# Kernel tuning notes

Hardware: AMD Instinct MI355X
Metric: run time of the kernel (lower is better)

The kernel has to match this reference:

```python
import jax, jax.numpy as jnp
import numpy as np

B = 16          # patients
V = 30          # max_visit
NV = 1501       # num_nodes + 1 (node vocab incl. padding)
NE = 2001       # num_edges + 1 (relation vocab incl. padding)
H = 128         # hidden_dim
D = 128         # start_embed_dim
L = 2           # gnn layers
OUT = 25        # out_dim
N_TOTAL = 100000  # concatenated graph nodes
E = 800000        # concatenated graph edges
DECAY = 0.01
EPS = 0.0       # self_attn


def setup_inputs() -> dict:
    key = jax.random.key(0)
    ks = jax.random.split(key, 16)
    s = 0.02
    return dict(
        node_emb_w=jax.random.normal(ks[0], (NV, D), jnp.float32) * s,
        edge_emb_w=jax.random.normal(ks[1], (NE, D), jnp.float32) * s,
        lin_w=jax.random.normal(ks[2], (H, D), jnp.float32) * s,
        lin_b=jnp.zeros((H,), jnp.float32),
        alpha_w=jax.random.normal(ks[3], (L, NV, NV), jnp.float32) * 0.01,
        alpha_b=jnp.zeros((L, NV), jnp.float32),
        beta_w=jax.random.normal(ks[4], (L, 1, NV), jnp.float32) * 0.01,
        beta_b=jnp.zeros((L, 1), jnp.float32),
        wr_w=jax.random.normal(ks[5], (L, 1, H), jnp.float32) * s,
        wr_b=jnp.zeros((L, 1), jnp.float32),
        conv_w=jax.random.normal(ks[6], (L, H, H), jnp.float32) * s,
        conv_b=jnp.zeros((L, H), jnp.float32),
        mlp_w=jax.random.normal(ks[7], (OUT, 2 * H), jnp.float32) * s,
        mlp_b=jnp.zeros((OUT,), jnp.float32),
        visit_node=jax.random.randint(ks[8], (B, V, NV), 0, 2).astype(jnp.int32),
        ehr_nodes=jax.random.randint(ks[9], (B, NV), 0, 2).astype(jnp.int32),
        cat_node_ids=jax.random.randint(ks[10], (N_TOTAL,), 1, NV).astype(jnp.int32),
        cat_edge_ids=jax.random.randint(ks[11], (E,), 1, NE).astype(jnp.int32),
        edge_index=jax.random.randint(ks[12], (2, E), 0, N_TOTAL).astype(jnp.int32),
        batch=jnp.repeat(jnp.arange(B, dtype=jnp.int32), N_TOTAL // B),
    )


def reference(node_emb_w, edge_emb_w, lin_w, lin_b, alpha_w, alpha_b,
              beta_w, beta_b, wr_w, wr_b, conv_w, conv_b, mlp_w, mlp_b,
              visit_node, ehr_nodes, cat_node_ids, cat_edge_ids, edge_index, batch):
    # lambda_j = exp(decay * (max_visit - j)), shape [1, V, 1]
    lam = jnp.exp(DECAY * (V - jnp.arange(V, dtype=jnp.float32)))[None, :, None]
    # embedding lookup + shared linear projection
    x = node_emb_w[cat_node_ids] @ lin_w.T + lin_b          # [N_total, H]
    eattr = edge_emb_w[cat_edge_ids] @ lin_w.T + lin_b      # [E, H]
    vn = visit_node.astype(jnp.float32)                     # [B, V, NV]
    src, dst = edge_index[0], edge_index[1]
    xj_nid = cat_node_ids[src]                               # [E]
    xj_b = batch[src]                                        # [E]
    for l in range(L):
        # visit-level attention: softmax over visits (dim=1)
        alpha = jax.nn.softmax(vn @ alpha_w[l].T + alpha_b[l], axis=1)   # [B,V,NV]
        beta = jnp.tanh(vn @ beta_w[l].T + beta_b[l]) * lam              # [B,V,1]
        attn = jnp.sum(alpha * beta, axis=1)                              # [B,NV]
        e_attn = attn[xj_b, xj_nid][:, None]                              # [E,1] per-edge gather
        # BiAttentionGNNConv: message = relu(x_j * attn * sigmoid(W_R e)), aggr=add
        w_rel = jax.nn.sigmoid(eattr @ wr_w[l].T + wr_b[l])               # [E,1]
        msg = jax.nn.relu(x[src] * e_attn * w_rel)                        # [E,H]
        agg = jax.ops.segment_sum(msg, dst, num_segments=N_TOTAL)        # scatter-add
        x = jax.nn.relu((agg + (1.0 + EPS) * x) @ conv_w[l].T + conv_b[l])
    # global mean pool over batch segments
    counts = jax.ops.segment_sum(jnp.ones((N_TOTAL,), jnp.float32), batch, num_segments=B)
    x_graph = jax.ops.segment_sum(x, batch, num_segments=B) / counts[:, None]
    # node branch: multi-hot average of node embeddings, then shared lin
    ehr = ehr_nodes.astype(jnp.float32)
    x_node = (ehr @ node_emb_w) / jnp.sum(ehr, axis=1, keepdims=True)
    x_node = x_node @ lin_w.T + lin_b
    return jnp.concatenate([x_graph, x_node], axis=1) @ mlp_w.T + mlp_b  # [B, OUT]
```

## Files before the change

### kernel.cpp

```cpp
#include <hip/hip_runtime.h>
#include <math.h>

namespace {
constexpr int kB = 16, kV = 30, kNV = 1501, kNE = 2001, kH = 128, kD = 128,
              kL = 2, kOut = 25, kNT = 100000, kE = 800000, kM = kB * kV;
constexpr int kKP = 1504;
constexpr int kKSZ = 4;
constexpr int kNVZ = 1536;
constexpr int kMZ = 512;
constexpr int kCAP = 32;
constexpr int kWrelBlocks = (kL * kNE + 255) / 256;
constexpr int kFuseB = kWrelBlocks + kMZ;
constexpr int kFuseTotal = kFuseB + kKP * kL;
}

typedef __attribute__((ext_vector_type(8))) short bfrag;
typedef __attribute__((ext_vector_type(4))) float ffrag;

__device__ inline unsigned short f2bf(float x) {
  unsigned u = __float_as_uint(x);
  unsigned r = u + 0x7FFFu + ((u >> 16) & 1u);
  return (unsigned short)(r >> 16);
}
__device__ inline float bf2f(unsigned short h) {
  return __uint_as_float(((unsigned)h) << 16);
}

__global__ void pn_kernel(const float* __restrict__ emb, const float* __restrict__ lw,
                          const float* __restrict__ lb, const float* __restrict__ cw,
                          const float* __restrict__ cb, float* __restrict__ pn,
                          float* __restrict__ pq2, float* __restrict__ ps,
                          float* __restrict__ accz) {
  int n = blockIdx.x, h = threadIdx.x;
  if (n == 0) {
    for (int i = h; i < 4128; i += kH) accz[i] = 0.f;
  }
  __shared__ float erow[kD];
  __shared__ float row[kD];
  erow[h] = emb[(size_t)n * kD + h];
  __syncthreads();
  float acc = lb[h];
#pragma unroll 8
  for (int d = 0; d < kD; d++) acc += erow[d] * lw[h * kD + d];
  pn[(size_t)n * kH + h] = acc;
  row[h] = acc;
  __syncthreads();
  float ap = 0.f, am = 0.f, aps = cb[h];
  const float* wr = cw + h * kD;
#pragma unroll 8
  for (int d = 0; d < kD; d++) {
    float r = row[d];
    float w = wr[d];
    ap = fmaf(fmaxf(r, 0.f), w, ap);
    am = fmaf(fmaxf(-r, 0.f), w, am);
    aps = fmaf(r, w, aps);
  }
  pq2[(size_t)n * kH + h] = ap;
  pq2[(size_t)(kNV + n) * kH + h] = am;
  ps[(size_t)n * kH + h] = aps;
}

__global__ void xnode_kernel(const int* __restrict__ ehr, const float* __restrict__ pn,
                             float* __restrict__ xacc, int* __restrict__ cnte) {
  int b = blockIdx.x;
  int c = blockIdx.y;
  int h = threadIdx.x;
  int n0 = c * 128;
  __shared__ int flags[128];
  int gn = n0 + h;
  flags[h] = (gn < kNV) ? ehr[(size_t)b * kNV + gn] : 0;
  __syncthreads();
  float acc = 0.f;
  int cnt = 0;
  int n1 = min(n0 + 128, kNV);
  for (int n = n0; n < n1; ++n) {
    if (flags[n - n0]) {
      acc += pn[(size_t)n * kH + h];
      cnt++;
    }
  }
  atomicAdd(&xacc[b * kH + h], acc);
  if (h == 0) atomicAdd(&cnte[b], cnt);
}

__global__ void front_kernel(const float* __restrict__ eemb, const float* __restrict__ wrw,
                             const float* __restrict__ wrb, const float* __restrict__ lw,
                             const float* __restrict__ lb, float* __restrict__ wrel,
                             const int* __restrict__ vn, short* __restrict__ out,
                             int* __restrict__ curz, const int* __restrict__ batch,
                             int* __restrict__ cnt, const float* __restrict__ bw,
                             const float* __restrict__ bb, float* __restrict__ beta,
                             const float* __restrict__ aw, short* __restrict__ awh) {
  const int blk = blockIdx.x;
  const int tid = threadIdx.x;
  if (blk < kWrelBlocks) {
    __shared__ float uc[258];
    {
      int l = tid >> 7, d = tid & 127;
      float s = 0.f;
      for (int h = 0; h < kH; h++) s += wrw[l * kH + h] * lw[h * kD + d];
      uc[tid] = s;
      if (tid < kL) {
        float c = wrb[tid];
        for (int h = 0; h < kH; h++) c += wrw[tid * kH + h] * lb[h];
        uc[256 + tid] = c;
      }
    }
    __syncthreads();
    int idx = blk * 256 + tid;
    if (idx >= kL * kNE) return;
    int l = idx / kNE, r = idx % kNE;
    float z = uc[256 + l];
    const float* u = uc + l * 128;
    const float* er = eemb + (size_t)r * kD;
    for (int d = 0; d < kD; d++) z += er[d] * u[d];
    wrel[idx] = 1.f / (1.f + expf(-z));
  } else if (blk < kFuseB) {
    int m = blk - kWrelBlocks;
    int b = m >> 5, v = m & 31;
    int gidx = m * 256 + tid;
    for (int i = gidx; i < 200000; i += 512 * 256) curz[i] = 0;
    __shared__ int bh[kB];
    __shared__ float rs[2][256];
    if (tid < kB) bh[tid] = 0;
    __syncthreads();
    if (gidx < kNT) atomicAdd(&bh[batch[gidx]], 1);
    __syncthreads();
    if (tid < kB && bh[tid]) atomicAdd(&cnt[tid], bh[tid]);
    float s0 = 0.f, s1 = 0.f;
    for (int k = tid; k < kKP; k += 256) {
      int val = (v < kV && k < kNV) ? vn[((size_t)(b * kV + v)) * kNV + k] : 0;
      out[(size_t)m * kKP + k] = val ? (short)0x3F80 : (short)0;
      if (val) {
        s0 += bw[k];
        s1 += bw[kNV + k];
      }
    }
    rs[0][tid] = s0;
    rs[1][tid] = s1;
    __syncthreads();
    for (int o = 128; o > 0; o >>= 1) {
      if (tid < o) {
        rs[0][tid] += rs[0][tid + o];
        rs[1][tid] += rs[1][tid + o];
      }
      __syncthreads();
    }
    if (tid == 0 && v < kV) {
      float lam = expf(0.01f * (float)(kV - v));
      beta[b * kV + v] = tanhf(rs[0][0] + bb[0]) * lam;
      beta[kM + b * kV + v] = tanhf(rs[1][0] + bb[1]) * lam;
    }
  } else {
    int id = blk - kFuseB;
    int n = id % kKP;
    int l = id / kKP;
    const size_t pl = (size_t)kKP * kKP;
    size_t rowo = ((size_t)l * kKP + n) * kKP;
    for (int k = tid; k < kKP; k += 256) {
      float x = (n < kNV && k < kNV) ? aw[((size_t)l * kNV + n) * kNV + k] : 0.f;
      unsigned short h1 = f2bf(x);
      float r1 = x - bf2f(h1);
      unsigned short h2 = f2bf(r1);
      float r2 = r1 - bf2f(h2);
      unsigned short h3 = f2bf(r2);
      awh[rowo + k] = (short)h1;
      awh[2 * pl + rowo + k] = (short)h2;
      awh[4 * pl + rowo + k] = (short)h3;
    }
  }
}

__global__ void zmfma_kernel(const short* __restrict__ vnbf, const short* __restrict__ awh,
                             float* __restrict__ zp) {
  const int l = blockIdx.z >> 2, ks = blockIdx.z & 3;
  const int wv = threadIdx.x >> 6, lane = threadIdx.x & 63;
  const int m0 = (blockIdx.y * 4 + wv) * 64;
  const int n0 = blockIdx.x * 32;
  const int lrow = lane & 15;
  const int koff = (lane >> 4) * 8;
  const size_t pl = (size_t)kKP * kKP;
  const short* p0 = awh + ((size_t)0 * 2 + l) * pl;
  const short* p1 = awh + ((size_t)1 * 2 + l) * pl;
  const short* p2 = awh + ((size_t)2 * 2 + l) * pl;
  ffrag acc[4][2];
#pragma unroll
  for (int i = 0; i < 4; ++i)
#pragma unroll
    for (int j = 0; j < 2; ++j) acc[i][j] = ffrag{0.f, 0.f, 0.f, 0.f};
  const int ct0 = ks * 12;
  const int ct1 = min(ct0 + 12, 47);
  for (int kt = ct0; kt < ct1; ++kt) {
    const int k = kt * 32 + koff;
    bfrag a0 = *(const bfrag*)(vnbf + (size_t)(m0 + 0 * 16 + lrow) * kKP + k);
    bfrag a1 = *(const bfrag*)(vnbf + (size_t)(m0 + 1 * 16 + lrow) * kKP + k);
    bfrag a2 = *(const bfrag*)(vnbf + (size_t)(m0 + 2 * 16 + lrow) * kKP + k);
    bfrag a3 = *(const bfrag*)(vnbf + (size_t)(m0 + 3 * 16 + lrow) * kKP + k);
    {
      bfrag b0 = *(const bfrag*)(p0 + (size_t)(n0 + lrow) * kKP + k);
      bfrag b1 = *(const bfrag*)(p0 + (size_t)(n0 + 16 + lrow) * kKP + k);
      acc[0][0] = __builtin_amdgcn_mfma_f32_16x16x32_bf16(a0, b0, acc[0][0], 0, 0, 0);
      acc[1][0] = __builtin_amdgcn_mfma_f32_16x16x32_bf16(a1, b0, acc[1][0], 0, 0, 0);
      acc[2][0] = __builtin_amdgcn_mfma_f32_16x16x32_bf16(a2, b0, acc[2][0], 0, 0, 0);
      acc[3][0] = __builtin_amdgcn_mfma_f32_16x16x32_bf16(a3, b0, acc[3][0], 0, 0, 0);
      acc[0][1] = __builtin_amdgcn_mfma_f32_16x16x32_bf16(a0, b1, acc[0][1], 0, 0, 0);
      acc[1][1] = __builtin_amdgcn_mfma_f32_16x16x32_bf16(a1, b1, acc[1][1], 0, 0, 0);
      acc[2][1] = __builtin_amdgcn_mfma_f32_16x16x32_bf16(a2, b1, acc[2][1], 0, 0, 0);
      acc[3][1] = __builtin_amdgcn_mfma_f32_16x16x32_bf16(a3, b1, acc[3][1], 0, 0, 0);
    }
    {
      bfrag b0 = *(const bfrag*)(p1 + (size_t)(n0 + lrow) * kKP + k);
      bfrag b1 = *(const bfrag*)(p1 + (size_t)(n0 + 16 + lrow) * kKP + k);
      acc[0][0] = __builtin_amdgcn_mfma_f32_16x16x32_bf16(a0, b0, acc[0][0], 0, 0, 0);
      acc[1][0] = __builtin_amdgcn_mfma_f32_16x16x32_bf16(a1, b0, acc[1][0], 0, 0, 0);
      acc[2][0] = __builtin_amdgcn_mfma_f32_16x16x32_bf16(a2, b0, acc[2][0], 0, 0, 0);
      acc[3][0] = __builtin_amdgcn_mfma_f32_16x16x32_bf16(a3, b0, acc[3][0], 0, 0, 0);
      acc[0][1] = __builtin_amdgcn_mfma_f32_16x16x32_bf16(a0, b1, acc[0][1], 0, 0, 0);
      acc[1][1] = __builtin_amdgcn_mfma_f32_16x16x32_bf16(a1, b1, acc[1][1], 0, 0, 0);
      acc[2][1] = __builtin_amdgcn_mfma_f32_16x16x32_bf16(a2, b1, acc[2][1], 0, 0, 0);
      acc[3][1] = __builtin_amdgcn_mfma_f32_16x16x32_bf16(a3, b1, acc[3][1], 0, 0, 0);
    }
    {
      bfrag b0 = *(const bfrag*)(p2 + (size_t)(n0 + lrow) * kKP + k);
      bfrag b1 = *(const bfrag*)(p2 + (size_t)(n0 + 16 + lrow) * kKP + k);
      acc[0][0] = __builtin_amdgcn_mfma_f32_16x16x32_bf16(a0, b0, acc[0][0], 0, 0, 0);
      acc[1][0] = __builtin_amdgcn_mfma_f32_16x16x32_bf16(a1, b0, acc[1][0], 0, 0, 0);
      acc[2][0] = __builtin_amdgcn_mfma_f32_16x16x32_bf16(a2, b0, acc[2][0], 0, 0, 0);
      acc[3][0] = __builtin_amdgcn_mfma_f32_16x16x32_bf16(a3, b0, acc[3][0], 0, 0, 0);
      acc[0][1] = __builtin_amdgcn_mfma_f32_16x16x32_bf16(a0, b1, acc[0][1], 0, 0, 0);
      acc[1][1] = __builtin_amdgcn_mfma_f32_16x16x32_bf16(a1, b1, acc[1][1], 0, 0, 0);
      acc[2][1] = __builtin_amdgcn_mfma_f32_16x16x32_bf16(a2, b1, acc[2][1], 0, 0, 0);
      acc[3][1] = __builtin_amdgcn_mfma_f32_16x16x32_bf16(a3, b1, acc[3][1], 0, 0, 0);
    }
  }
  const int drow0 = (lane >> 4) * 4;
  float* zb = zp + (size_t)(ks * kL + l) * kMZ * kNVZ;
#pragma unroll
  for (int i = 0; i < 4; ++i) {
    int mrow = m0 + i * 16 + drow0;
#pragma unroll
    for (int j = 0; j < 2; ++j) {
      int ncol = n0 + j * 16 + lrow;
#pragma unroll
      for (int r = 0; r < 4; ++r) zb[(size_t)(mrow + r) * kNVZ + ncol] = acc[i][j][r];
    }
  }
}

__global__ void zsm_kernel(const float* __restrict__ zp, const float* __restrict__ beta,
                           float* __restrict__ attn) {
  int idx = blockIdx.x * blockDim.x + threadIdx.x;
  if (idx >= kL * kB * kNV) return;
  int n = idx % kNV;
  int lb_ = idx / kNV;
  int l = lb_ / kB, b = lb_ % kB;
  const size_t PSTR = (size_t)kL * kMZ * kNVZ;
  const float* p = zp + ((size_t)l * kMZ + b * 32) * kNVZ + n;
  float zz[kV];
  float m = -1e30f;
#pragma unroll
  for (int v = 0; v < kV; ++v) {
    size_t o = (size_t)v * kNVZ;
    float s = p[o] + p[o + PSTR] + p[o + 2 * PSTR] + p[o + 3 * PSTR];
    zz[v] = s;
    m = fmaxf(m, s);
  }
  float s = 0.f, num = 0.f;
  const float* bet = beta + lb_ * kV;
#pragma unroll
  for (int v = 0; v < kV; ++v) {
    float e = expf(zz[v] - m);
    s += e;
    num += e * bet[v];
  }
  attn[idx] = num / s;
}

__global__ void scatter_kernel(const int* __restrict__ ei, const int* __restrict__ nid,
                               const int* __restrict__ eid, const int* __restrict__ batch,
                               const float* __restrict__ attn, const float* __restrict__ wrel,
                               int* __restrict__ cnt1, unsigned short* __restrict__ csnb,
                               float* __restrict__ cs0b, int* __restrict__ cnt2,
                               int* __restrict__ csrs2b, float* __restrict__ cs1cb) {
  int e = blockIdx.x * blockDim.x + threadIdx.x;
  if (e >= kE) return;
  int s = ei[e], d = ei[kE + e];
  int b = batch[s], n = nid[s], r = eid[e];
  float a0 = attn[(size_t)b * kNV + n];
  float a1 = attn[(size_t)kB * kNV + b * kNV + n];
  float w0 = wrel[r], w1 = wrel[kNE + r];
  int pos = atomicAdd(&cnt1[d], 1);
  if (pos < kCAP) {
    csnb[(size_t)d * kCAP + pos] = (unsigned short)(n + ((a0 > 0.f) ? 0 : kNV));
    cs0b[(size_t)d * kCAP + pos] = fabsf(a0) * w0;
  }
  if (a1 > 0.f) {
    int p2 = atomicAdd(&cnt2[d], 1);
    if (p2 < kCAP) {
      csrs2b[(size_t)d * kCAP + p2] = s;
      cs1cb[(size_t)d * kCAP + p2] = a1 * w1;
    }
  }
}

#define GACC(A, V, C)                                  \
  A.x = fmaf(V.x, C, A.x); A.y = fmaf(V.y, C, A.y);    \
  A.z = fmaf(V.z, C, A.z); A.w = fmaf(V.w, C, A.w);

__global__ void l1_kernel(const float* __restrict__ pq2, const float* __restrict__ psTab,
                          const int* __restrict__ nid, const unsigned short* __restrict__ csn,
                          const float* __restrict__ cs0, const int* __restrict__ cnt1,
                          float* __restrict__ xa) {
  const int tid = threadIdx.x;
  const int lane = tid & 63;
  const int sub = lane >> 5, sl = lane & 31;
  const int hw = (tid >> 6) * 2 + sub;
  int node = blockIdx.x * 16 + hw;
  if (node >= kNT) return;
  const float4* x4 = (const float4*)pq2;
  float4 a0 = ((const float4*)psTab)[(size_t)nid[node] * 32 + sl];
  float4 a1 = {0.f, 0.f, 0.f, 0.f};
  float4 a2 = {0.f, 0.f, 0.f, 0.f};
  float4 a3 = {0.f, 0.f, 0.f, 0.f};
  int j0 = node * kCAP;
  int j1 = j0 + min(cnt1[node], kCAP);
  for (int base = j0; base < j1; base += 32) {
    int n = j1 - base;
    if (n > 32) n = 32;
    int sidx = 0;
    float ssc = 0.f;
    if (sl < n) {
      sidx = (int)csn[base + sl];
      ssc = cs0[base + sl];
    }
    int t = 0;
    for (; t + 8 <= n; t += 8) {
      int s0 = __shfl(sidx, sub * 32 + t + 0, 64);
      int s1 = __shfl(sidx, sub * 32 + t + 1, 64);
      int s2 = __shfl(sidx, sub * 32 + t + 2, 64);
      int s3 = __shfl(sidx, sub * 32 + t + 3, 64);
      int s4i = __shfl(sidx, sub * 32 + t + 4, 64);
      int s5 = __shfl(sidx, sub * 32 + t + 5, 64);
      int s6 = __shfl(sidx, sub * 32 + t + 6, 64);
      int s7 = __shfl(sidx, sub * 32 + t + 7, 64);
      float c0 = __shfl(ssc, sub * 32 + t + 0, 64);
      float c1 = __shfl(ssc, sub * 32 + t + 1, 64);
      float c2 = __shfl(ssc, sub * 32 + t + 2, 64);
      float c3 = __shfl(ssc, sub * 32 + t + 3, 64);
      float c4 = __shfl(ssc, sub * 32 + t + 4, 64);
      float c5 = __shfl(ssc, sub * 32 + t + 5, 64);
      float c6 = __shfl(ssc, sub * 32 + t + 6, 64);
      float c7 = __shfl(ssc, sub * 32 + t + 7, 64);
      float4 v0 = x4[(size_t)s0 * 32 + sl];
      float4 v1 = x4[(size_t)s1 * 32 + sl];
      float4 v2 = x4[(size_t)s2 * 32 + sl];
      float4 v3 = x4[(size_t)s3 * 32 + sl];
      float4 v4 = x4[(size_t)s4i * 32 + sl];
      float4 v5 = x4[(size_t)s5 * 32 + sl];
      float4 v6 = x4[(size_t)s6 * 32 + sl];
      float4 v7 = x4[(size_t)s7 * 32 + sl];
      GACC(a0, v0, c0);
      GACC(a1, v1, c1);
      GACC(a2, v2, c2);
      GACC(a3, v3, c3);
      GACC(a0, v4, c4);
      GACC(a1, v5, c5);
      GACC(a2, v6, c6);
      GACC(a3, v7, c7);
    }
    for (; t + 4 <= n; t += 4) {
      int s0 = __shfl(sidx, sub * 32 + t + 0, 64);
      int s1 = __shfl(sidx, sub * 32 + t + 1, 64);
      int s2 = __shfl(sidx, sub * 32 + t + 2, 64);
      int s3 = __shfl(sidx, sub * 32 + t + 3, 64);
      float c0 = __shfl(ssc, sub * 32 + t + 0, 64);
      float c1 = __shfl(ssc, sub * 32 + t + 1, 64);
      float c2 = __shfl(ssc, sub * 32 + t + 2, 64);
      float c3 = __shfl(ssc, sub * 32 + t + 3, 64);
      float4 v0 = x4[(size_t)s0 * 32 + sl];
      float4 v1 = x4[(size_t)s1 * 32 + sl];
      float4 v2 = x4[(size_t)s2 * 32 + sl];
      float4 v3 = x4[(size_t)s3 * 32 + sl];
      GACC(a0, v0, c0);
      GACC(a1, v1, c1);
      GACC(a2, v2, c2);
      GACC(a3, v3, c3);
    }
    for (; t < n; ++t) {
      int s = __shfl(sidx, sub * 32 + t, 64);
      float sc = __shfl(ssc, sub * 32 + t, 64);
      float4 xv = x4[(size_t)s * 32 + sl];
      GACC(a0, xv, sc);
    }
  }
  float4 o;
  o.x = fmaxf(a0.x + a1.x + a2.x + a3.x, 0.f);
  o.y = fmaxf(a0.y + a1.y + a2.y + a3.y, 0.f);
  o.z = fmaxf(a0.z + a1.z + a2.z + a3.z, 0.f);
  o.w = fmaxf(a0.w + a1.w + a2.w + a3.w, 0.f);
  ((float4*)xa)[(size_t)node * 32 + sl] = o;
}

template <int POOL>
__global__ void gconv_kernel(const float* __restrict__ srcTab,
                             const float* __restrict__ selfTab,
                             const int* __restrict__ cidx, const float* __restrict__ cscal,
                             const int* __restrict__ cnt, const int* __restrict__ selfIdx,
                             const float* __restrict__ w, const float* __restrict__ bias,
                             float* __restrict__ xout, float* __restrict__ xg,
                             const int* __restrict__ batch) {
  const int nb = blockIdx.x * 64;
  const int tid = threadIdx.x;
  __shared__ float As[128 * 64];
  __shared__ float Ws[32 * 132];
  const int wv = tid >> 6;
  const int lane = tid & 63;
  const int sub = lane >> 5, sl = lane & 31;
  const int hw = wv * 2 + sub;
  const float4* x4 = (const float4*)srcTab;
  const float4* s4 = (const float4*)selfTab;
  int nct[4];
  float4 selfa[4];
#pragma unroll
  for (int p = 0; p < 4; ++p) {
    int node = nb + p * 16 + hw;
    if (node < kNT) {
      nct[p] = min(cnt[node], kCAP);
      int selfRow = selfIdx ? selfIdx[node] : node;
      selfa[p] = s4[(size_t)selfRow * 32 + sl];
    } else {
      nct[p] = 0;
      selfa[p] = float4{0.f, 0.f, 0.f, 0.f};
    }
  }
  int sidxr[4];
  float sscr[4];
#pragma unroll
  for (int p = 0; p < 4; ++p) {
    int node = nb + p * 16 + hw;
    sidxr[p] = 0;
    sscr[p] = 0.f;
    if (node < kNT && sl < nct[p]) {
      size_t jb = (size_t)node * kCAP;
      sidxr[p] = cidx[jb + sl];
      sscr[p] = cscal[jb + sl];
    }
  }
#pragma unroll
  for (int p = 0; p < 4; ++p) {
    int nl = p * 16 + hw;
    int node = nb + nl;
    if (node < kNT) {
      float4 a0 = selfa[p];
      float4 a1 = {0.f, 0.f, 0.f, 0.f};
      float4 a2 = {0.f, 0.f, 0.f, 0.f};
      float4 a3 = {0.f, 0.f, 0.f, 0.f};
      int n = nct[p];
      int sidx = sidxr[p];
      float ssc = sscr[p];
      int t = 0;
      for (; t + 8 <= n; t += 8) {
        int s0 = __shfl(sidx, sub * 32 + t + 0, 64);
        int s1 = __shfl(sidx, sub * 32 + t + 1, 64);
        int s2 = __shfl(sidx, sub * 32 + t + 2, 64);
        int s3 = __shfl(sidx, sub * 32 + t + 3, 64);
        int s4i = __shfl(sidx, sub * 32 + t + 4, 64);
        int s5 = __shfl(sidx, sub * 32 + t + 5, 64);
        int s6 = __shfl(sidx, sub * 32 + t + 6, 64);
        int s7 = __shfl(sidx, sub * 32 + t + 7, 64);
        float c0 = __shfl(ssc, sub * 32 + t + 0, 64);
        float c1 = __shfl(ssc, sub * 32 + t + 1, 64);
        float c2 = __shfl(ssc, sub * 32 + t + 2, 64);
        float c3 = __shfl(ssc, sub * 32 + t + 3, 64);
        float c4 = __shfl(ssc, sub * 32 + t + 4, 64);
        float c5 = __shfl(ssc, sub * 32 + t + 5, 64);
        float c6 = __shfl(ssc, sub * 32 + t + 6, 64);
        float c7 = __shfl(ssc, sub * 32 + t + 7, 64);
        float4 v0 = x4[(size_t)s0 * 32 + sl];
        float4 v1 = x4[(size_t)s1 * 32 + sl];
        float4 v2 = x4[(size_t)s2 * 32 + sl];
        float4 v3 = x4[(size_t)s3 * 32 + sl];
        float4 v4 = x4[(size_t)s4i * 32 + sl];
        float4 v5 = x4[(size_t)s5 * 32 + sl];
        float4 v6 = x4[(size_t)s6 * 32 + sl];
        float4 v7 = x4[(size_t)s7 * 32 + sl];
        GACC(a0, v0, c0);
        GACC(a1, v1, c1);
        GACC(a2, v2, c2);
        GACC(a3, v3, c3);
        GACC(a0, v4, c4);
        GACC(a1, v5, c5);
        GACC(a2, v6, c6);
        GACC(a3, v7, c7);
      }
      for (; t + 4 <= n; t += 4) {
        int s0 = __shfl(sidx, sub * 32 + t + 0, 64);
        int s1 = __shfl(sidx, sub * 32 + t + 1, 64);
        int s2 = __shfl(sidx, sub * 32 + t + 2, 64);
        int s3 = __shfl(sidx, sub * 32 + t + 3, 64);
        float c0 = __shfl(ssc, sub * 32 + t + 0, 64);
        float c1 = __shfl(ssc, sub * 32 + t + 1, 64);
        float c2 = __shfl(ssc, sub * 32 + t + 2, 64);
        float c3 = __shfl(ssc, sub * 32 + t + 3, 64);
        float4 v0 = x4[(size_t)s0 * 32 + sl];
        float4 v1 = x4[(size_t)s1 * 32 + sl];
        float4 v2 = x4[(size_t)s2 * 32 + sl];
        float4 v3 = x4[(size_t)s3 * 32 + sl];
        GACC(a0, v0, c0);
        GACC(a1, v1, c1);
        GACC(a2, v2, c2);
        GACC(a3, v3, c3);
      }
      for (; t < n; ++t) {
        int s = __shfl(sidx, sub * 32 + t, 64);
        float sc = __shfl(ssc, sub * 32 + t, 64);
        float4 xv = x4[(size_t)s * 32 + sl];
        GACC(a0, xv, sc);
      }
      float av[4] = {a0.x + a1.x + a2.x + a3.x, a0.y + a1.y + a2.y + a3.y,
                     a0.z + a1.z + a2.z + a3.z, a0.w + a1.w + a2.w + a3.w};
#pragma unroll
      for (int j = 0; j < 4; ++j) {
        int d = sl * 4 + j;
        int g = (nl >> 2) ^ (sl & 15);
        As[d * 64 + (g << 2) + (nl & 3)] = av[j];
      }
    }
  }
  __syncthreads();
  const int tx = tid & 31, ty = tid >> 5;
  const int n0 = tx * 4;
  float acc[4][4] = {};
  for (int kc = 0; kc < 4; ++kc) {
    if (kc) __syncthreads();
#pragma unroll
    for (int i = 0; i < 2; ++i) {
      int fi = tid + i * 512;
      int hh = fi >> 3, c4 = (fi & 7) * 4;
      float4 v = *(const float4*)(w + (size_t)hh * kD + kc * 32 + c4);
      Ws[(c4 + 0) * 132 + hh] = v.x;
      Ws[(c4 + 1) * 132 + hh] = v.y;
      Ws[(c4 + 2) * 132 + hh] = v.z;
      Ws[(c4 + 3) * 132 + hh] = v.w;
    }
    __syncthreads();
#pragma unroll
    for (int dd = 0; dd < 32; ++dd) {
      int d = kc * 32 + dd;
      float4 a = *(const float4*)&As[d * 64 + ((ty ^ ((d >> 2) & 15)) << 2)];
      float4 b0 = *(const float4*)&Ws[dd * 132 + n0];
      float am[4] = {a.x, a.y, a.z, a.w};
      float bn[4] = {b0.x, b0.y, b0.z, b0.w};
#pragma unroll
      for (int i2 = 0; i2 < 4; ++i2)
#pragma unroll
        for (int j2 = 0; j2 < 4; ++j2) acc[i2][j2] += am[i2] * bn[j2];
    }
  }
  float4 bv0 = *(const float4*)(bias + n0);
  float bb[4] = {bv0.x, bv0.y, bv0.z, bv0.w};
  if (POOL == 0) {
#pragma unroll
    for (int i2 = 0; i2 < 4; ++i2) {
      int r = nb + ty * 4 + i2;
      if (r < kNT) {
        float4 o0;
        o0.x = fmaxf(acc[i2][0] + bb[0], 0.f);
        o0.y = fmaxf(acc[i2][1] + bb[1], 0.f);
        o0.z = fmaxf(acc[i2][2] + bb[2], 0.f);
        o0.w = fmaxf(acc[i2][3] + bb[3], 0.f);
        *(float4*)(xout + (size_t)r * kH + n0) = o0;
      }
    }
  } else {
    int rlast = min(nb + 63, kNT - 1);
    int b0 = batch[nb], b1v = batch[rlast];
    if (b0 == b1v) {
      float p[4] = {};
#pragma unroll
      for (int i2 = 0; i2 < 4; ++i2) {
        int r = nb + ty * 4 + i2;
        if (r < kNT) {
#pragma unroll
          for (int j2 = 0; j2 < 4; ++j2) p[j2] += fmaxf(acc[i2][j2] + bb[j2], 0.f);
        }
      }
      __syncthreads();
      float* Ls = Ws;
#pragma unroll
      for (int j2 = 0; j2 < 4; ++j2) Ls[ty * 132 + n0 + j2] = p[j2];
      __syncthreads();
      if (tid < 128) {
        float s = 0.f;
#pragma unroll
        for (int r2 = 0; r2 < 16; ++r2) s += Ls[r2 * 132 + tid];
        atomicAdd(&xg[b0 * kH + tid], s);
      }
    } else {
#pragma unroll
      for (int i2 = 0; i2 < 4; ++i2) {
        int r = nb + ty * 4 + i2;
        if (r < kNT) {
          int br = batch[r];
#pragma unroll
          for (int j2 = 0; j2 < 4; ++j2)
            atomicAdd(&xg[br * kH + n0 + j2], fmaxf(acc[i2][j2] + bb[j2], 0.f));
        }
      }
    }
  }
}

__global__ void final_kernel(const float* __restrict__ xg, const int* __restrict__ cnt,
                             const float* __restrict__ xacc, const int* __restrict__ cnte,
                             const float* __restrict__ mw, const float* __restrict__ mb,
                             float* __restrict__ out) {
  int idx = blockIdx.x * blockDim.x + threadIdx.x;
  if (idx >= kB * kOut) return;
  int b = idx / kOut, o = idx % kOut;
  float invg = 1.f / (float)cnt[b];
  float invn = 1.f / (float)cnte[b];
  float acc = mb[o];
  const float* w = mw + (size_t)o * (2 * kH);
  for (int h = 0; h < kH; h++) acc += xg[b * kH + h] * invg * w[h];
  for (int h = 0; h < kH; h++) acc += xacc[b * kH + h] * invn * w[kH + h];
  out[idx] = acc;
}

extern "C" void kernel_launch(void* const* d_in, const int* in_sizes, int n_in,
                              void* d_out, int out_size, void* d_ws, size_t ws_size,
                              hipStream_t stream) {
  const float* node_emb = (const float*)d_in[0];
  const float* edge_emb = (const float*)d_in[1];
  const float* lin_w = (const float*)d_in[2];
  const float* lin_b = (const float*)d_in[3];
  const float* alpha_w = (const float*)d_in[4];
  const float* alpha_b = (const float*)d_in[5];
  const float* beta_w = (const float*)d_in[6];
  const float* beta_b = (const float*)d_in[7];
  const float* wr_w = (const float*)d_in[8];
  const float* wr_b = (const float*)d_in[9];
  const float* conv_w = (const float*)d_in[10];
  const float* conv_b = (const float*)d_in[11];
  const float* mlp_w = (const float*)d_in[12];
  const float* mlp_b = (const float*)d_in[13];
  const int* visit_node = (const int*)d_in[14];
  const int* ehr_nodes = (const int*)d_in[15];
  const int* cat_node_ids = (const int*)d_in[16];
  const int* cat_edge_ids = (const int*)d_in[17];
  const int* edge_index = (const int*)d_in[18];
  const int* batch = (const int*)d_in[19];

  char* ws = (char*)d_ws;
  float* ZP = (float*)(ws);
  float* XA = (float*)(ws);
  float* PN = (float*)(ws + 51200000);
  short* VNBF = (short*)(ws + 52000000);
  float* PQ2 = (float*)(ws + 53600000);
  float* PS = (float*)(ws + 55200000);
  short* AWH = (short*)(ws + 56000000);
  unsigned short* CSNB = (unsigned short*)(ws + 56000000);
  float* CS0B = (float*)(ws + 62400000);
  float* ATTN = (float*)(ws + 83200000);
  float* BETA = (float*)(ws + 83400000);
  float* WREL = (float*)(ws + 83410000);
  int* CNT1 = (int*)(ws + 83500000);
  int* CNT2 = (int*)(ws + 83900000);
  int* CSRS2B = (int*)(ws + 84300000);
  float* CS1CB = (float*)(ws + 97100000);
  float* XG = (float*)(ws + 109900000);
  int* CNT = (int*)(ws + 109908192);
  float* XNACC = (float*)(ws + 109908256);
  int* CNTE = (int*)(ws + 109916448);

  pn_kernel<<<kNV, kH, 0, stream>>>(node_emb, lin_w, lin_b, conv_w, conv_b, PN, PQ2, PS, XG);
  xnode_kernel<<<dim3(kB, 12), kH, 0, stream>>>(ehr_nodes, PN, XNACC, CNTE);
  front_kernel<<<kFuseTotal, 256, 0, stream>>>(edge_emb, wr_w, wr_b, lin_w, lin_b, WREL,
                                               visit_node, VNBF, CNT1, batch, CNT, beta_w,
                                               beta_b, BETA, alpha_w, AWH);
  zmfma_kernel<<<dim3(47, 2, kL * kKSZ), 256, 0, stream>>>(VNBF, AWH, ZP);
  zsm_kernel<<<(kL * kB * kNV + 255) / 256, 256, 0, stream>>>(ZP, BETA, ATTN);

  scatter_kernel<<<(kE + 255) / 256, 256, 0, stream>>>(edge_index, cat_node_ids, cat_edge_ids,
                                                       batch, ATTN, WREL, CNT1, CSNB, CS0B,
                                                       CNT2, CSRS2B, CS1CB);

  l1_kernel<<<(kNT + 15) / 16, 512, 0, stream>>>(PQ2, PS, cat_node_ids, CSNB, CS0B, CNT1, XA);
  gconv_kernel<1><<<(kNT + 63) / 64, 512, 0, stream>>>(XA, XA, CSRS2B, CS1CB, CNT2, nullptr,
                                                       conv_w + (size_t)kH * kD, conv_b + kH,
                                                       nullptr, XG, batch);

  final_kernel<<<2, 256, 0, stream>>>(XG, CNT, XNACC, CNTE, mlp_w, mlp_b, (float*)d_out);
}
```

Before: 293.0 us.

## Fold pn and xnode kernels into front kernel and reassociate node branch

Moves the per-node projection (pq2/ps) and the node-branch multi-hot sum into extra block ranges of the front kernel, removing two launches and the PN buffer. The node branch now sums raw embeddings and applies lin_w through a precomputed mlp_w·lin_w product in the final kernel. Partial sums are stored per block instead of accumulated atomically. The batch histogram moves into extra blocks of the zsm kernel. This removes launch overhead and serialization but changes the floating-point summation order.

```diff
diff --git a/kernel.cpp b/kernel.cpp
--- a/kernel.cpp
+++ b/kernel.cpp
@@ -10,8 +10,17 @@
 constexpr int kMZ = 512;
 constexpr int kCAP = 32;
 constexpr int kWrelBlocks = (kL * kNE + 255) / 256;
-constexpr int kFuseB = kWrelBlocks + kMZ;
-constexpr int kFuseTotal = kFuseB + kKP * kL;
+constexpr int kVnBase = kWrelBlocks;
+constexpr int kAwBase = kVnBase + kMZ;
+constexpr int kPnBase = kAwBase + kKP * kL;
+constexpr int kPnBlocks = (kNV + 1) / 2;
+constexpr int kXnBase = kPnBase + kPnBlocks;
+constexpr int kXnBlocks = kB * 12;
+constexpr int kMwBase = kXnBase + kXnBlocks;
+constexpr int kMwBlocks = (kOut * kD + 255) / 256;
+constexpr int kFrontTotal = kMwBase + kMwBlocks;
+constexpr int kZsmBlocks = (kL * kB * kNV + 255) / 256;
+constexpr int kCntBlocks = (kNT + 255) / 256;
 }
 
 typedef __attribute__((ext_vector_type(8))) short bfrag;
@@ -26,71 +35,20 @@
   return __uint_as_float(((unsigned)h) << 16);
 }
 
-__global__ void pn_kernel(const float* __restrict__ emb, const float* __restrict__ lw,
-                          const float* __restrict__ lb, const float* __restrict__ cw,
-                          const float* __restrict__ cb, float* __restrict__ pn,
-                          float* __restrict__ pq2, float* __restrict__ ps,
-                          float* __restrict__ accz) {
-  int n = blockIdx.x, h = threadIdx.x;
-  if (n == 0) {
-    for (int i = h; i < 4128; i += kH) accz[i] = 0.f;
-  }
-  __shared__ float erow[kD];
-  __shared__ float row[kD];
-  erow[h] = emb[(size_t)n * kD + h];
-  __syncthreads();
-  float acc = lb[h];
-#pragma unroll 8
-  for (int d = 0; d < kD; d++) acc += erow[d] * lw[h * kD + d];
-  pn[(size_t)n * kH + h] = acc;
-  row[h] = acc;
-  __syncthreads();
-  float ap = 0.f, am = 0.f, aps = cb[h];
-  const float* wr = cw + h * kD;
-#pragma unroll 8
-  for (int d = 0; d < kD; d++) {
-    float r = row[d];
-    float w = wr[d];
-    ap = fmaf(fmaxf(r, 0.f), w, ap);
-    am = fmaf(fmaxf(-r, 0.f), w, am);
-    aps = fmaf(r, w, aps);
-  }
-  pq2[(size_t)n * kH + h] = ap;
-  pq2[(size_t)(kNV + n) * kH + h] = am;
-  ps[(size_t)n * kH + h] = aps;
-}
-
-__global__ void xnode_kernel(const int* __restrict__ ehr, const float* __restrict__ pn,
-                             float* __restrict__ xacc, int* __restrict__ cnte) {
-  int b = blockIdx.x;
-  int c = blockIdx.y;
-  int h = threadIdx.x;
-  int n0 = c * 128;
-  __shared__ int flags[128];
-  int gn = n0 + h;
-  flags[h] = (gn < kNV) ? ehr[(size_t)b * kNV + gn] : 0;
-  __syncthreads();
-  float acc = 0.f;
-  int cnt = 0;
-  int n1 = min(n0 + 128, kNV);
-  for (int n = n0; n < n1; ++n) {
-    if (flags[n - n0]) {
-      acc += pn[(size_t)n * kH + h];
-      cnt++;
-    }
-  }
-  atomicAdd(&xacc[b * kH + h], acc);
-  if (h == 0) atomicAdd(&cnte[b], cnt);
-}
-
 __global__ void front_kernel(const float* __restrict__ eemb, const float* __restrict__ wrw,
                              const float* __restrict__ wrb, const float* __restrict__ lw,
                              const float* __restrict__ lb, float* __restrict__ wrel,
                              const int* __restrict__ vn, short* __restrict__ out,
-                             int* __restrict__ curz, const int* __restrict__ batch,
-                             int* __restrict__ cnt, const float* __restrict__ bw,
+                             int* __restrict__ curz, const float* __restrict__ bw,
                              const float* __restrict__ bb, float* __restrict__ beta,
-                             const float* __restrict__ aw, short* __restrict__ awh) {
+                             const float* __restrict__ aw, short* __restrict__ awh,
+                             const float* __restrict__ emb, const float* __restrict__ cw,
+                             const float* __restrict__ cb, float* __restrict__ pq2,
+                             float* __restrict__ ps, const int* __restrict__ ehr,
+                             float* __restrict__ xnpart, int* __restrict__ cntep,
+                             const float* __restrict__ mw, float* __restrict__ mlpw2,
+                             float* __restrict__ lbdot, float* __restrict__ xg,
+                             int* __restrict__ cntg) {
   const int blk = blockIdx.x;
   const int tid = threadIdx.x;
   if (blk < kWrelBlocks) {
@@ -115,18 +73,16 @@
     const float* er = eemb + (size_t)r * kD;
     for (int d = 0; d < kD; d++) z += er[d] * u[d];
     wrel[idx] = 1.f / (1.f + expf(-z));
-  } else if (blk < kFuseB) {
-    int m = blk - kWrelBlocks;
+  } else if (blk < kAwBase) {
+    int m = blk - kVnBase;
     int b = m >> 5, v = m & 31;
     int gidx = m * 256 + tid;
     for (int i = gidx; i < 200000; i += 512 * 256) curz[i] = 0;
-    __shared__ int bh[kB];
+    if (m == 0) {
+      for (int i = tid; i < kB * kH; i += 256) xg[i] = 0.f;
+      if (tid < kB) cntg[tid] = 0;
+    }
     __shared__ float rs[2][256];
-    if (tid < kB) bh[tid] = 0;
-    __syncthreads();
-    if (gidx < kNT) atomicAdd(&bh[batch[gidx]], 1);
-    __syncthreads();
-    if (tid < kB && bh[tid]) atomicAdd(&cnt[tid], bh[tid]);
     float s0 = 0.f, s1 = 0.f;
     for (int k = tid; k < kKP; k += 256) {
       int val = (v < kV && k < kNV) ? vn[((size_t)(b * kV + v)) * kNV + k] : 0;
@@ -151,8 +107,8 @@
       beta[b * kV + v] = tanhf(rs[0][0] + bb[0]) * lam;
       beta[kM + b * kV + v] = tanhf(rs[1][0] + bb[1]) * lam;
     }
-  } else {
-    int id = blk - kFuseB;
+  } else if (blk < kPnBase) {
+    int id = blk - kAwBase;
     int n = id % kKP;
     int l = id / kKP;
     const size_t pl = (size_t)kKP * kKP;
@@ -167,6 +123,76 @@
       awh[rowo + k] = (short)h1;
       awh[2 * pl + rowo + k] = (short)h2;
       awh[4 * pl + rowo + k] = (short)h3;
+    }
+  } else if (blk < kXnBase) {
+    int id = blk - kPnBase;
+    int half = tid >> 7;
+    int h = tid & 127;
+    int n = id * 2 + half;
+    bool valid = n < kNV;
+    __shared__ float erow[2][128];
+    __shared__ float row[2][128];
+    erow[half][h] = valid ? emb[(size_t)n * kD + h] : 0.f;
+    __syncthreads();
+    float acc = lb[h];
+#pragma unroll 8
+    for (int d = 0; d < kD; d++) acc += erow[half][d] * lw[h * kD + d];
+    row[half][h] = acc;
+    __syncthreads();
+    float ap = 0.f, am = 0.f, aps = cb[h];
+    const float* wr = cw + h * kD;
+#pragma unroll 8
+    for (int d = 0; d < kD; d++) {
+      float r = row[half][d];
+      float w = wr[d];
+      ap = fmaf(fmaxf(r, 0.f), w, ap);
+      am = fmaf(fmaxf(-r, 0.f), w, am);
+      aps = fmaf(r, w, aps);
+    }
+    if (valid) {
+      pq2[(size_t)n * kH + h] = ap;
+      pq2[(size_t)(kNV + n) * kH + h] = am;
+      ps[(size_t)n * kH + h] = aps;
+    }
+  } else if (blk < kMwBase) {
+    int id = blk - kXnBase;
+    int b = id / 12, c = id % 12;
+    int half = tid >> 7;
+    int h = tid & 127;
+    int n0 = c * 128;
+    __shared__ int flags[128];
+    __shared__ float red[256];
+    if (tid < 128) {
+      int gn = n0 + tid;
+      flags[tid] = (gn < kNV) ? ehr[(size_t)b * kNV + gn] : 0;
+    }
+    __syncthreads();
+    float acc = 0.f;
+    int nlo = n0 + half * 64;
+    int nhi = min(nlo + 64, kNV);
+    for (int n = nlo; n < nhi; ++n) {
+      if (flags[n - n0]) acc += emb[(size_t)n * kD + h];
+    }
+    red[tid] = acc;
+    __syncthreads();
+    if (tid < 128) xnpart[(size_t)id * kH + tid] = red[tid] + red[128 + tid];
+    if (tid == 0) {
+      int ct = 0;
+      for (int i = 0; i < 128; ++i) ct += flags[i] ? 1 : 0;
+      cntep[id] = ct;
+    }
+  } else {
+    int gid = (blk - kMwBase) * 256 + tid;
+    if (gid < kOut * kD) {
+      int o = gid >> 7, d = gid & 127;
+      float s = 0.f;
+      for (int h = 0; h < kH; h++) s += mw[(size_t)o * (2 * kH) + kH + h] * lw[h * kD + d];
+      mlpw2[gid] = s;
+    }
+    if (gid < kOut) {
+      float s = 0.f;
+      for (int h = 0; h < kH; h++) s += lb[h] * mw[(size_t)gid * (2 * kH) + kH + h];
+      lbdot[gid] = s;
     }
   }
 }
@@ -248,7 +274,18 @@
 }
 
 __global__ void zsm_kernel(const float* __restrict__ zp, const float* __restrict__ beta,
-                           float* __restrict__ attn) {
+                           float* __restrict__ attn, const int* __restrict__ batch,
+                           int* __restrict__ cntg) {
+  if (blockIdx.x >= kZsmBlocks) {
+    int i = (blockIdx.x - kZsmBlocks) * 256 + threadIdx.x;
+    __shared__ int bh[kB];
+    if (threadIdx.x < kB) bh[threadIdx.x] = 0;
+    __syncthreads();
+    if (i < kNT) atomicAdd(&bh[batch[i]], 1);
+    __syncthreads();
+    if (threadIdx.x < kB && bh[threadIdx.x]) atomicAdd(&cntg[threadIdx.x], bh[threadIdx.x]);
+    return;
+  }
   int idx = blockIdx.x * blockDim.x + threadIdx.x;
   if (idx >= kL * kB * kNV) return;
   int n = idx % kNV;
@@ -611,20 +648,39 @@
   }
 }
 
-__global__ void final_kernel(const float* __restrict__ xg, const int* __restrict__ cnt,
-                             const float* __restrict__ xacc, const int* __restrict__ cnte,
+__global__ void final_kernel(const float* __restrict__ xg, const int* __restrict__ cntg,
+                             const float* __restrict__ xnp, const int* __restrict__ cntep,
+                             const float* __restrict__ mlpw2, const float* __restrict__ lbdot,
                              const float* __restrict__ mw, const float* __restrict__ mb,
                              float* __restrict__ out) {
-  int idx = blockIdx.x * blockDim.x + threadIdx.x;
-  if (idx >= kB * kOut) return;
-  int b = idx / kOut, o = idx % kOut;
-  float invg = 1.f / (float)cnt[b];
-  float invn = 1.f / (float)cnte[b];
-  float acc = mb[o];
+  const int tid = threadIdx.x;
+  __shared__ float xn[kB * kH];
+  __shared__ float ce[kB];
+  for (int i = tid; i < kB * kH; i += 512) {
+    int b = i >> 7, d = i & 127;
+    float s = 0.f;
+    for (int c = 0; c < 12; ++c) s += xnp[(size_t)(b * 12 + c) * kH + d];
+    xn[i] = s;
+  }
+  if (tid < kB) {
+    int s = 0;
+    for (int c = 0; c < 12; ++c) s += cntep[tid * 12 + c];
+    ce[tid] = (float)s;
+  }
+  __syncthreads();
+  if (tid >= kB * kOut) return;
+  int b = tid / kOut, o = tid % kOut;
+  float invg = 1.f / (float)cntg[b];
+  float invn = 1.f / ce[b];
+  float acc = mb[o] + lbdot[o];
   const float* w = mw + (size_t)o * (2 * kH);
-  for (int h = 0; h < kH; h++) acc += xg[b * kH + h] * invg * w[h];
-  for (int h = 0; h < kH; h++) acc += xacc[b * kH + h] * invn * w[kH + h];
-  out[idx] = acc;
+  float s1 = 0.f;
+  for (int h = 0; h < kH; h++) s1 += xg[b * kH + h] * w[h];
+  acc += invg * s1;
+  float s2 = 0.f;
+  for (int d = 0; d < kD; d++) s2 += xn[b * kH + d] * mlpw2[o * kD + d];
+  acc += invn * s2;
+  out[tid] = acc;
 }
 
 extern "C" void kernel_launch(void* const* d_in, const int* in_sizes, int n_in,
@@ -654,7 +710,6 @@
   char* ws = (char*)d_ws;
   float* ZP = (float*)(ws);
   float* XA = (float*)(ws);
-  float* PN = (float*)(ws + 51200000);
   short* VNBF = (short*)(ws + 52000000);
   float* PQ2 = (float*)(ws + 53600000);
   float* PS = (float*)(ws + 55200000);
@@ -670,16 +725,17 @@
   float* CS1CB = (float*)(ws + 97100000);
   float* XG = (float*)(ws + 109900000);
   int* CNT = (int*)(ws + 109908192);
-  float* XNACC = (float*)(ws + 109908256);
-  int* CNTE = (int*)(ws + 109916448);
-
-  pn_kernel<<<kNV, kH, 0, stream>>>(node_emb, lin_w, lin_b, conv_w, conv_b, PN, PQ2, PS, XG);
-  xnode_kernel<<<dim3(kB, 12), kH, 0, stream>>>(ehr_nodes, PN, XNACC, CNTE);
-  front_kernel<<<kFuseTotal, 256, 0, stream>>>(edge_emb, wr_w, wr_b, lin_w, lin_b, WREL,
-                                               visit_node, VNBF, CNT1, batch, CNT, beta_w,
-                                               beta_b, BETA, alpha_w, AWH);
+  float* XNPART = (float*)(ws + 109920000);
+  int* CNTEP = (int*)(ws + 110020000);
+  float* MLPW2 = (float*)(ws + 110021000);
+  float* LBDOT = (float*)(ws + 110034000);
+
+  front_kernel<<<kFrontTotal, 256, 0, stream>>>(
+      edge_emb, wr_w, wr_b, lin_w, lin_b, WREL, visit_node, VNBF, CNT1, beta_w, beta_b, BETA,
+      alpha_w, AWH, node_emb, conv_w, conv_b, PQ2, PS, ehr_nodes, XNPART, CNTEP, mlp_w, MLPW2,
+      LBDOT, XG, CNT);
   zmfma_kernel<<<dim3(47, 2, kL * kKSZ), 256, 0, stream>>>(VNBF, AWH, ZP);
-  zsm_kernel<<<(kL * kB * kNV + 255) / 256, 256, 0, stream>>>(ZP, BETA, ATTN);
+  zsm_kernel<<<kZsmBlocks + kCntBlocks, 256, 0, stream>>>(ZP, BETA, ATTN, batch, CNT);
 
   scatter_kernel<<<(kE + 255) / 256, 256, 0, stream>>>(edge_index, cat_node_ids, cat_edge_ids,
                                                        batch, ATTN, WREL, CNT1, CSNB, CS0B,
@@ -690,5 +746,6 @@
                                                        conv_w + (size_t)kH * kD, conv_b + kH,
                                                        nullptr, XG, batch);
 
-  final_kernel<<<2, 256, 0, stream>>>(XG, CNT, XNACC, CNTE, mlp_w, mlp_b, (float*)d_out);
-}
+  final_kernel<<<1, 512, 0, stream>>>(XG, CNT, XNPART, CNTEP, MLPW2, LBDOT, mlp_w, mlp_b,
+                                      (float*)d_out);
+}
```

Result: faster. 286.1 us (-2.3%).
